# Optimization experiments

Measured on AMD Instinct MI355X. Metric: run time of the kernel, lower is better.

The kernel has to match this reference:

```python
import jax, jax.numpy as jnp
import numpy as np

RANK = 8
ALPHA = 8.0 / RANK  # module stores alpha/rank


def setup_inputs() -> dict:
    key = jax.random.key(0)
    k1, k2, k3, k4, k5 = jax.random.split(key, 5)
    M, N = 4096, 4096          # out_features, in_features
    T = 8192                   # flattened batch*seq tokens
    x = jax.random.normal(k1, (T, N), dtype=jnp.float32)
    W = jax.random.normal(k2, (M, N), dtype=jnp.float32) * 0.02
    b = jax.random.normal(k3, (M,), dtype=jnp.float32) * 0.02
    A = jax.random.normal(k4, (M, RANK), dtype=jnp.float32) * 0.01
    B = jax.random.normal(k5, (N, RANK), dtype=jnp.float32) * 0.01
    return {"x": x, "W": W, "b": b, "A": A, "B": B}


def reference(x, W, b, A, B):
    # Faithful to the torch module: delta_W = alpha * (A @ B.T) is materialized
    # [M, N], then out = linear(x) + F.linear(x, delta_W).
    delta_W = ALPHA * (A @ B.T)                 # [M, N]
    return x @ W.T + b + x @ delta_W.T          # [T, M]
```

## Files before the change

kernel.cpp:

```cpp
#include <hip/hip_runtime.h>
#include <hip/hip_bf16.h>
#include <cstdint>
#include <cstddef>


#define T_DIM 8192
#define M_DIM 4096
#define N_DIM 4096
#define RANK  8

typedef _Float16 f16x8 __attribute__((ext_vector_type(8)));
typedef float    f32x4 __attribute__((ext_vector_type(4)));

__global__ __launch_bounds__(256)
void fuse_x(const float* __restrict__ x, const float* __restrict__ B,
            _Float16* __restrict__ xh, float* __restrict__ xB) {
    __shared__ float sred[4][8];
    const int t   = blockIdx.x;
    const int tid = threadIdx.x;

    {
        const int n0 = tid * 16;
        const float* xrow = x + (size_t)t * N_DIM + n0;
        f32x4 xv[4];
#pragma unroll
        for (int k = 0; k < 4; ++k) xv[k] = *(const f32x4*)(xrow + k * 4);
        f16x8 h0, h1;
#pragma unroll
        for (int k = 0; k < 4; ++k) { h0[k] = (_Float16)xv[0][k]; h0[4 + k] = (_Float16)xv[1][k]; }
#pragma unroll
        for (int k = 0; k < 4; ++k) { h1[k] = (_Float16)xv[2][k]; h1[4 + k] = (_Float16)xv[3][k]; }
        *(f16x8*)(xh + (size_t)t * N_DIM + n0)     = h0;
        *(f16x8*)(xh + (size_t)t * N_DIM + n0 + 8) = h1;
    }

    f32x4 acc0 = {0.f, 0.f, 0.f, 0.f}, acc1 = {0.f, 0.f, 0.f, 0.f};
    const float* xrow = x + (size_t)t * N_DIM;
#pragma unroll
    for (int k = 0; k < 16; ++k) {
        const int n = k * 256 + tid;
        const float xs = xrow[n];
        const float* Brow = B + (size_t)n * RANK;
        f32x4 b0 = *(const f32x4*)(Brow);
        f32x4 b1 = *(const f32x4*)(Brow + 4);
        acc0 += xs * b0;
        acc1 += xs * b1;
    }

    float v[8];
#pragma unroll
    for (int k = 0; k < 4; ++k) { v[k] = acc0[k]; v[4 + k] = acc1[k]; }
#pragma unroll
    for (int off = 32; off > 0; off >>= 1)
#pragma unroll
        for (int k = 0; k < 8; ++k) v[k] += __shfl_down(v[k], off);
    const int lane = tid & 63, wave = tid >> 6;
    if (lane == 0)
#pragma unroll
        for (int k = 0; k < 8; ++k) sred[wave][k] = v[k];
    __syncthreads();
    if (tid < 8)
        xB[(size_t)t * RANK + tid] =
            sred[0][tid] + sred[1][tid] + sred[2][tid] + sred[3][tid];
}

__global__ __launch_bounds__(256)
void cvt_f16(const float* __restrict__ src, _Float16* __restrict__ dst) {
    size_t i = ((size_t)blockIdx.x * blockDim.x + threadIdx.x) * 8;
    f32x4 v0 = *(const f32x4*)(src + i);
    f32x4 v1 = *(const f32x4*)(src + i + 4);
    f16x8 o;
#pragma unroll
    for (int k = 0; k < 4; ++k) { o[k] = (_Float16)v0[k]; o[4 + k] = (_Float16)v1[k]; }
    *(f16x8*)(dst + i) = o;
}

__device__ static inline void gld_lds16(const void* g, void* l) {
    __builtin_amdgcn_global_load_lds(
        (const __attribute__((address_space(1))) unsigned int*)g,
        (__attribute__((address_space(3))) unsigned int*)l, 16, 0, 0);
}

__global__ __launch_bounds__(256, 2)
void gemm_f16(const _Float16* __restrict__ X, const _Float16* __restrict__ Wt,
              const float* __restrict__ bias, const float* __restrict__ A,
              const float* __restrict__ xB, float* __restrict__ out) {
    __shared__ __align__(16) _Float16 lA[128 * 32];
    __shared__ __align__(16) _Float16 lB[128 * 32];

    const int tid  = threadIdx.x;
    const int lane = tid & 63;
    const int wave = tid >> 6;
    const int wr = wave >> 1, wc = wave & 1;
    const int bx = blockIdx.x, by = blockIdx.y;

    const size_t rowX0 = (size_t)by * 128;
    const size_t rowW0 = (size_t)bx * 128;

    const int srow = tid >> 2;
    const int scol = (tid & 3) << 3;
    const int fr = lane & 15;
    const int fk = (lane >> 4) << 3;

    f32x4 acc[4][4] = {};

    for (int k0 = 0; k0 < N_DIM; k0 += 32) {
        gld_lds16(X  + (rowX0      + srow) * N_DIM + k0 + scol, &lA[tid * 8]);
        gld_lds16(X  + (rowX0 + 64 + srow) * N_DIM + k0 + scol, &lA[2048 + tid * 8]);
        gld_lds16(Wt + (rowW0      + srow) * N_DIM + k0 + scol, &lB[tid * 8]);
        gld_lds16(Wt + (rowW0 + 64 + srow) * N_DIM + k0 + scol, &lB[2048 + tid * 8]);
        asm volatile("s_waitcnt vmcnt(0)" ::: "memory");
        __syncthreads();

        f16x8 af[4], bf[4];
#pragma unroll
        for (int i = 0; i < 4; ++i)
            af[i] = *(const f16x8*)&lA[(wr * 64 + i * 16 + fr) * 32 + fk];
#pragma unroll
        for (int i = 0; i < 4; ++i)
            bf[i] = *(const f16x8*)&lB[(wc * 64 + i * 16 + fr) * 32 + fk];
#pragma unroll
        for (int i = 0; i < 4; ++i)
#pragma unroll
            for (int j = 0; j < 4; ++j)
                acc[i][j] = __builtin_amdgcn_mfma_f32_16x16x32_f16(
                    af[i], bf[j], acc[i][j], 0, 0, 0);
        __syncthreads();
    }

    const int crow0 = by * 128 + wr * 64;
    const int ccol0 = bx * 128 + wc * 64;

    f32x4 Ac0[4], Ac1[4];
    float bv[4];
    int   colv[4];
#pragma unroll
    for (int j = 0; j < 4; ++j) {
        const int col = ccol0 + j * 16 + (lane & 15);
        colv[j] = col;
        bv[j]   = bias[col];
        Ac0[j]  = *(const f32x4*)(A + (size_t)col * RANK);
        Ac1[j]  = *(const f32x4*)(A + (size_t)col * RANK + 4);
    }
#pragma unroll
    for (int i = 0; i < 4; ++i) {
#pragma unroll
        for (int r = 0; r < 4; ++r) {
            const int row = crow0 + i * 16 + ((lane >> 4) << 2) + r;
            f32x4 xb0 = *(const f32x4*)(xB + (size_t)row * RANK);
            f32x4 xb1 = *(const f32x4*)(xB + (size_t)row * RANK + 4);
#pragma unroll
            for (int j = 0; j < 4; ++j) {
                float d = xb0[0] * Ac0[j][0] + xb0[1] * Ac0[j][1]
                        + xb0[2] * Ac0[j][2] + xb0[3] * Ac0[j][3]
                        + xb1[0] * Ac1[j][0] + xb1[1] * Ac1[j][1]
                        + xb1[2] * Ac1[j][2] + xb1[3] * Ac1[j][3];
                out[(size_t)row * M_DIM + colv[j]] = acc[i][j][r] + bv[j] + d;
            }
        }
    }
}

extern "C" void kernel_launch(void* const* d_in, const int* in_sizes, int n_in,
                              void* d_out, int out_size, void* d_ws, size_t ws_size,
                              hipStream_t stream) {
    const float* x = (const float*)d_in[0];
    const float* W = (const float*)d_in[1];
    const float* b = (const float*)d_in[2];
    const float* A = (const float*)d_in[3];
    const float* B = (const float*)d_in[4];
    float* out = (float*)d_out;

    _Float16* Wh = (_Float16*)d_ws;
    _Float16* Xh = (_Float16*)((char*)d_ws + (size_t)M_DIM * N_DIM * 2);
    float*    xB = (float*)   ((char*)d_ws + (size_t)M_DIM * N_DIM * 2
                                           + (size_t)T_DIM * N_DIM * 2);

    fuse_x<<<T_DIM, 256, 0, stream>>>(x, B, Xh, xB);
    cvt_f16<<<((size_t)M_DIM * N_DIM / 8) / 256, 256, 0, stream>>>(W, Wh);

    dim3 grid(M_DIM / 128, T_DIM / 128);
    gemm_f16<<<grid, dim3(256, 1, 1), 0, stream>>>(Xh, Wh, b, A, xB, out);
}
```

Measured before the change: 626.8 us.

## Fold LoRA delta into fp16 weights and use pipelined 256x256 GEMM

```diff
diff --git a/kernel.cpp b/kernel.cpp
--- a/kernel.cpp
+++ b/kernel.cpp
@@ -1,5 +1,4 @@
 #include <hip/hip_runtime.h>
-#include <hip/hip_bf16.h>
 #include <cstdint>
 #include <cstddef>
 
@@ -13,59 +12,7 @@
 typedef float    f32x4 __attribute__((ext_vector_type(4)));
 
 __global__ __launch_bounds__(256)
-void fuse_x(const float* __restrict__ x, const float* __restrict__ B,
-            _Float16* __restrict__ xh, float* __restrict__ xB) {
-    __shared__ float sred[4][8];
-    const int t   = blockIdx.x;
-    const int tid = threadIdx.x;
-
-    {
-        const int n0 = tid * 16;
-        const float* xrow = x + (size_t)t * N_DIM + n0;
-        f32x4 xv[4];
-#pragma unroll
-        for (int k = 0; k < 4; ++k) xv[k] = *(const f32x4*)(xrow + k * 4);
-        f16x8 h0, h1;
-#pragma unroll
-        for (int k = 0; k < 4; ++k) { h0[k] = (_Float16)xv[0][k]; h0[4 + k] = (_Float16)xv[1][k]; }
-#pragma unroll
-        for (int k = 0; k < 4; ++k) { h1[k] = (_Float16)xv[2][k]; h1[4 + k] = (_Float16)xv[3][k]; }
-        *(f16x8*)(xh + (size_t)t * N_DIM + n0)     = h0;
-        *(f16x8*)(xh + (size_t)t * N_DIM + n0 + 8) = h1;
-    }
-
-    f32x4 acc0 = {0.f, 0.f, 0.f, 0.f}, acc1 = {0.f, 0.f, 0.f, 0.f};
-    const float* xrow = x + (size_t)t * N_DIM;
-#pragma unroll
-    for (int k = 0; k < 16; ++k) {
-        const int n = k * 256 + tid;
-        const float xs = xrow[n];
-        const float* Brow = B + (size_t)n * RANK;
-        f32x4 b0 = *(const f32x4*)(Brow);
-        f32x4 b1 = *(const f32x4*)(Brow + 4);
-        acc0 += xs * b0;
-        acc1 += xs * b1;
-    }
-
-    float v[8];
-#pragma unroll
-    for (int k = 0; k < 4; ++k) { v[k] = acc0[k]; v[4 + k] = acc1[k]; }
-#pragma unroll
-    for (int off = 32; off > 0; off >>= 1)
-#pragma unroll
-        for (int k = 0; k < 8; ++k) v[k] += __shfl_down(v[k], off);
-    const int lane = tid & 63, wave = tid >> 6;
-    if (lane == 0)
-#pragma unroll
-        for (int k = 0; k < 8; ++k) sred[wave][k] = v[k];
-    __syncthreads();
-    if (tid < 8)
-        xB[(size_t)t * RANK + tid] =
-            sred[0][tid] + sred[1][tid] + sred[2][tid] + sred[3][tid];
-}
-
-__global__ __launch_bounds__(256)
-void cvt_f16(const float* __restrict__ src, _Float16* __restrict__ dst) {
+void cast_x(const float* __restrict__ src, _Float16* __restrict__ dst) {
     size_t i = ((size_t)blockIdx.x * blockDim.x + threadIdx.x) * 8;
     f32x4 v0 = *(const f32x4*)(src + i);
     f32x4 v1 = *(const f32x4*)(src + i + 4);
@@ -75,90 +22,172 @@
     *(f16x8*)(dst + i) = o;
 }
 
-__device__ static inline void gld_lds16(const void* g, void* l) {
+__global__ __launch_bounds__(256)
+void prep_w(const float* __restrict__ W, const float* __restrict__ A,
+            const float* __restrict__ B, _Float16* __restrict__ Wh) {
+    const size_t c = (size_t)blockIdx.x * 256 + threadIdx.x;
+    const int m  = (int)(c >> 9);
+    const int n0 = (int)(c & 511) << 3;
+    f32x4 a0 = *(const f32x4*)(A + (size_t)m * RANK);
+    f32x4 a1 = *(const f32x4*)(A + (size_t)m * RANK + 4);
+    const float* wp = W + (size_t)m * N_DIM + n0;
+    f32x4 w0 = *(const f32x4*)wp;
+    f32x4 w1 = *(const f32x4*)(wp + 4);
+    f16x8 o;
+#pragma unroll
+    for (int k = 0; k < 8; ++k) {
+        const float* Bn = B + (size_t)(n0 + k) * RANK;
+        f32x4 b0 = *(const f32x4*)Bn;
+        f32x4 b1 = *(const f32x4*)(Bn + 4);
+        float d = a0[0]*b0[0] + a0[1]*b0[1] + a0[2]*b0[2] + a0[3]*b0[3]
+                + a1[0]*b1[0] + a1[1]*b1[1] + a1[2]*b1[2] + a1[3]*b1[3];
+        float wv = (k < 4) ? w0[k] : w1[k - 4];
+        o[k] = (_Float16)(wv + d);
+    }
+    *(f16x8*)(Wh + (size_t)m * N_DIM + n0) = o;
+}
+
+__device__ static inline void gld16(const _Float16* g, _Float16* l) {
     __builtin_amdgcn_global_load_lds(
         (const __attribute__((address_space(1))) unsigned int*)g,
         (__attribute__((address_space(3))) unsigned int*)l, 16, 0, 0);
 }
 
-__global__ __launch_bounds__(256, 2)
-void gemm_f16(const _Float16* __restrict__ X, const _Float16* __restrict__ Wt,
-              const float* __restrict__ bias, const float* __restrict__ A,
-              const float* __restrict__ xB, float* __restrict__ out) {
-    __shared__ __align__(16) _Float16 lA[128 * 32];
-    __shared__ __align__(16) _Float16 lB[128 * 32];
+__global__ __launch_bounds__(512, 2)
+void gemm256(const _Float16* __restrict__ Xh, const _Float16* __restrict__ Wh,
+             const float* __restrict__ bias, float* __restrict__ out) {
+    __shared__ __align__(16) _Float16 lA[2][256 * 64];
+    __shared__ __align__(16) _Float16 lB[2][256 * 64];
 
     const int tid  = threadIdx.x;
     const int lane = tid & 63;
-    const int wave = tid >> 6;
-    const int wr = wave >> 1, wc = wave & 1;
-    const int bx = blockIdx.x, by = blockIdx.y;
-
-    const size_t rowX0 = (size_t)by * 128;
-    const size_t rowW0 = (size_t)bx * 128;
-
-    const int srow = tid >> 2;
-    const int scol = (tid & 3) << 3;
-    const int fr = lane & 15;
-    const int fk = (lane >> 4) << 3;
-
-    f32x4 acc[4][4] = {};
-
-    for (int k0 = 0; k0 < N_DIM; k0 += 32) {
-        gld_lds16(X  + (rowX0      + srow) * N_DIM + k0 + scol, &lA[tid * 8]);
-        gld_lds16(X  + (rowX0 + 64 + srow) * N_DIM + k0 + scol, &lA[2048 + tid * 8]);
-        gld_lds16(Wt + (rowW0      + srow) * N_DIM + k0 + scol, &lB[tid * 8]);
-        gld_lds16(Wt + (rowW0 + 64 + srow) * N_DIM + k0 + scol, &lB[2048 + tid * 8]);
-        asm volatile("s_waitcnt vmcnt(0)" ::: "memory");
-        __syncthreads();
-
-        f16x8 af[4], bf[4];
-#pragma unroll
-        for (int i = 0; i < 4; ++i)
-            af[i] = *(const f16x8*)&lA[(wr * 64 + i * 16 + fr) * 32 + fk];
-#pragma unroll
-        for (int i = 0; i < 4; ++i)
-            bf[i] = *(const f16x8*)&lB[(wc * 64 + i * 16 + fr) * 32 + fk];
-#pragma unroll
-        for (int i = 0; i < 4; ++i)
+    const int fr   = lane & 15;
+    const int fq   = lane >> 4;
+    const int w    = tid >> 6;
+    const int wr   = w >> 2;
+    const int wcn  = w & 3;
+
+    const size_t rowX0 = (size_t)blockIdx.y * 256;
+    const size_t rowW0 = (size_t)blockIdx.x * 256;
+
+    const int srow = tid >> 3;
+    const int scol = ((tid & 7) * 8) ^ ((srow & 7) * 8);
+    const _Float16* sA = Xh + (rowX0 + srow) * N_DIM + scol;
+    const _Float16* sBp[4];
+#pragma unroll
+    for (int cb = 0; cb < 4; ++cb) {
+        const int p = cb * 64 + srow;
+        const int wrow = ((p >> 5) & 3) * 64 + ((p >> 7) & 1) * 32 + (p & 31);
+        sBp[cb] = Wh + (rowW0 + wrow) * N_DIM + scol;
+    }
+
+    const int kc0 = (fq * 8) ^ ((fr & 7) * 8);
+
+    f32x4 acc[8][4] = {};
+    f16x8 af[4][2], bf[4][2];
+
+#define STAGE_A(b, rb, kt) gld16(sA + (size_t)(rb) * N_DIM + (kt) * 64, \
+                                 &lA[b][(rb) * 64 + tid * 8])
+#define STAGE_B(b, cb, kt) gld16(sBp[cb] + (size_t)(kt) * 64, \
+                                 &lB[b][(cb) * 4096 + tid * 8])
+
+#define LDA(b, qm) do { _Pragma("unroll") \
+    for (int ii = 0; ii < 4; ++ii) { \
+        const int ro_ = (wr * 128 + (qm) * 64 + ii * 16 + fr) * 64; \
+        af[ii][0] = *(const f16x8*)&lA[b][ro_ + kc0]; \
+        af[ii][1] = *(const f16x8*)&lA[b][ro_ + (kc0 ^ 32)]; } } while (0)
+
+#define LDB(b, qn) do { _Pragma("unroll") \
+    for (int jj = 0; jj < 2; ++jj) { \
+        const int ro_ = ((qn) * 128 + wcn * 32 + jj * 16 + fr) * 64; \
+        bf[(qn) * 2 + jj][0] = *(const f16x8*)&lB[b][ro_ + kc0]; \
+        bf[(qn) * 2 + jj][1] = *(const f16x8*)&lB[b][ro_ + (kc0 ^ 32)]; } } while (0)
+
+#define MMA(qm, qn) do { __builtin_amdgcn_s_setprio(1); \
+    _Pragma("unroll") for (int ii = 0; ii < 4; ++ii) \
+    _Pragma("unroll") for (int jj = 0; jj < 2; ++jj) { \
+        acc[(qm)*4+ii][(qn)*2+jj] = __builtin_amdgcn_mfma_f32_16x16x32_f16( \
+            af[ii][0], bf[(qn)*2+jj][0], acc[(qm)*4+ii][(qn)*2+jj], 0, 0, 0); \
+        acc[(qm)*4+ii][(qn)*2+jj] = __builtin_amdgcn_mfma_f32_16x16x32_f16( \
+            af[ii][1], bf[(qn)*2+jj][1], acc[(qm)*4+ii][(qn)*2+jj], 0, 0, 0); } \
+    __builtin_amdgcn_s_setprio(0); \
+    __builtin_amdgcn_sched_barrier(0); } while (0)
+
+#define BAR asm volatile("s_barrier" ::: "memory")
+#define VW4 asm volatile("s_waitcnt vmcnt(4)" ::: "memory")
+#define VW0 asm volatile("s_waitcnt vmcnt(0)" ::: "memory")
+
+    STAGE_A(0, 0, 0);   STAGE_A(0, 128, 0);  STAGE_B(0, 0, 0);  STAGE_B(0, 1, 0);
+    STAGE_A(0, 64, 0);  STAGE_A(0, 192, 0);  STAGE_B(0, 2, 0);  STAGE_B(0, 3, 0);
+    STAGE_A(1, 0, 1);   STAGE_A(1, 128, 1);  STAGE_B(1, 0, 1);  STAGE_B(1, 1, 1);
+    VW4; BAR;
+
+#pragma unroll 1
+    for (int n = 0; n < (N_DIM / 128) - 1; ++n) {
+        const int ko  = 2 * n + 1;
+        const int kne = 2 * n + 2;
+        const int kno = 2 * n + 3;
+        LDA(0, 0); LDB(0, 0);
+        STAGE_A(1, 64, ko); STAGE_A(1, 192, ko); STAGE_B(1, 2, ko); STAGE_B(1, 3, ko);
+        BAR; MMA(0, 0); BAR;
+        LDB(0, 1);
+        BAR; MMA(0, 1); BAR;
+        LDA(0, 1); STAGE_A(0, 0, kne); STAGE_A(0, 128, kne);
+        BAR; MMA(1, 0); BAR;
+        STAGE_B(0, 0, kne); STAGE_B(0, 1, kne);
+        BAR; MMA(1, 1); VW4; BAR;
+        LDA(1, 0); LDB(1, 0); STAGE_A(0, 64, kne); STAGE_A(0, 192, kne);
+        BAR; MMA(0, 0); BAR;
+        LDB(1, 1); STAGE_B(0, 2, kne); STAGE_B(0, 3, kne);
+        BAR; MMA(0, 1); BAR;
+        LDA(1, 1); STAGE_A(1, 0, kno); STAGE_A(1, 128, kno);
+        BAR; MMA(1, 0); BAR;
+        STAGE_B(1, 0, kno); STAGE_B(1, 1, kno);
+        BAR; MMA(1, 1); VW4; BAR;
+    }
+
+    {
+        const int ko = N_DIM / 64 - 1;
+        LDA(0, 0); LDB(0, 0);
+        STAGE_A(1, 64, ko); STAGE_A(1, 192, ko); STAGE_B(1, 2, ko); STAGE_B(1, 3, ko);
+        BAR; MMA(0, 0); BAR;
+        LDB(0, 1);
+        BAR; MMA(0, 1); BAR;
+        LDA(0, 1);
+        BAR; MMA(1, 0); BAR;
+        BAR; MMA(1, 1); VW0; BAR;
+        LDA(1, 0); LDB(1, 0);
+        BAR; MMA(0, 0); BAR;
+        LDB(1, 1);
+        BAR; MMA(0, 1); BAR;
+        LDA(1, 1);
+        BAR; MMA(1, 0); BAR;
+        MMA(1, 1);
+    }
+
+    const int crow0 = (int)rowX0 + wr * 128;
+    const int ccol0 = (int)rowW0 + wcn * 64;
+    float bv[4];
+#pragma unroll
+    for (int j = 0; j < 4; ++j) bv[j] = bias[ccol0 + j * 16 + fr];
+#pragma unroll
+    for (int i = 0; i < 8; ++i) {
+#pragma unroll
+        for (int r = 0; r < 4; ++r) {
+            const size_t row = (size_t)(crow0 + i * 16 + fq * 4 + r);
 #pragma unroll
             for (int j = 0; j < 4; ++j)
-                acc[i][j] = __builtin_amdgcn_mfma_f32_16x16x32_f16(
-                    af[i], bf[j], acc[i][j], 0, 0, 0);
-        __syncthreads();
-    }
-
-    const int crow0 = by * 128 + wr * 64;
-    const int ccol0 = bx * 128 + wc * 64;
-
-    f32x4 Ac0[4], Ac1[4];
-    float bv[4];
-    int   colv[4];
-#pragma unroll
-    for (int j = 0; j < 4; ++j) {
-        const int col = ccol0 + j * 16 + (lane & 15);
-        colv[j] = col;
-        bv[j]   = bias[col];
-        Ac0[j]  = *(const f32x4*)(A + (size_t)col * RANK);
-        Ac1[j]  = *(const f32x4*)(A + (size_t)col * RANK + 4);
-    }
-#pragma unroll
-    for (int i = 0; i < 4; ++i) {
-#pragma unroll
-        for (int r = 0; r < 4; ++r) {
-            const int row = crow0 + i * 16 + ((lane >> 4) << 2) + r;
-            f32x4 xb0 = *(const f32x4*)(xB + (size_t)row * RANK);
-            f32x4 xb1 = *(const f32x4*)(xB + (size_t)row * RANK + 4);
-#pragma unroll
-            for (int j = 0; j < 4; ++j) {
-                float d = xb0[0] * Ac0[j][0] + xb0[1] * Ac0[j][1]
-                        + xb0[2] * Ac0[j][2] + xb0[3] * Ac0[j][3]
-                        + xb1[0] * Ac1[j][0] + xb1[1] * Ac1[j][1]
-                        + xb1[2] * Ac1[j][2] + xb1[3] * Ac1[j][3];
-                out[(size_t)row * M_DIM + colv[j]] = acc[i][j][r] + bv[j] + d;
-            }
+                out[row * M_DIM + ccol0 + j * 16 + fr] = acc[i][j][r] + bv[j];
         }
     }
+#undef STAGE_A
+#undef STAGE_B
+#undef LDA
+#undef LDB
+#undef MMA
+#undef BAR
+#undef VW4
+#undef VW0
 }
 
 extern "C" void kernel_launch(void* const* d_in, const int* in_sizes, int n_in,
@@ -173,12 +202,10 @@
 
     _Float16* Wh = (_Float16*)d_ws;
     _Float16* Xh = (_Float16*)((char*)d_ws + (size_t)M_DIM * N_DIM * 2);
-    float*    xB = (float*)   ((char*)d_ws + (size_t)M_DIM * N_DIM * 2
-                                           + (size_t)T_DIM * N_DIM * 2);
-
-    fuse_x<<<T_DIM, 256, 0, stream>>>(x, B, Xh, xB);
-    cvt_f16<<<((size_t)M_DIM * N_DIM / 8) / 256, 256, 0, stream>>>(W, Wh);
-
-    dim3 grid(M_DIM / 128, T_DIM / 128);
-    gemm_f16<<<grid, dim3(256, 1, 1), 0, stream>>>(Xh, Wh, b, A, xB, out);
-}
+
+    cast_x<<<((size_t)T_DIM * N_DIM / 8) / 256, 256, 0, stream>>>(x, Xh);
+    prep_w<<<((size_t)M_DIM * N_DIM / 8) / 256, 256, 0, stream>>>(W, A, B, Wh);
+
+    dim3 grid(M_DIM / 256, T_DIM / 256);
+    gemm256<<<grid, dim3(512, 1, 1), 0, stream>>>(Xh, Wh, b, out);
+}
```

Result: faster. 562.8 us (-10.2%).
